# Performance work log

Measured on AMD Instinct MI355X. Metric: run time of the kernel, lower is better.

## Reference

```python
import jax, jax.numpy as jnp
import numpy as np

D_MODEL = 512
D_ALPHA = 100
D_PH = 80
SCALE = 1.0 / np.sqrt(D_MODEL)


def gru_cell(x, h, Wih, Whh, bih, bhh):
    # PyTorch GRU gate order: r, z, n
    gi = x @ Wih.T + bih
    gh = h @ Whh.T + bhh
    ir, iz, inn = jnp.split(gi, 3, axis=-1)
    hr, hz, hn = jnp.split(gh, 3, axis=-1)
    r = jax.nn.sigmoid(ir + hr)
    z = jax.nn.sigmoid(iz + hz)
    n = jnp.tanh(inn + r * hn)
    return (1.0 - z) * n + z * h


def attend(q, k, v):
    # q: [B,D], k/v: [B,L,D]
    scores = jnp.einsum('bd,bld->bl', q, k) * SCALE
    a = jax.nn.softmax(scores, axis=-1)  # [B,L]
    o = jnp.einsum('bl,bld->bd', a, v)
    return a, o


def setup_inputs() -> dict:
    key = jax.random.key(0)
    ks = jax.random.split(key, 25)
    D = D_MODEL

    def u(k, shape, fan):
        return jax.random.uniform(k, shape, jnp.float32, -1.0, 1.0) / np.sqrt(fan)

    inp = {
        'text': jax.random.randint(ks[0], (256, 128), 0, D_ALPHA),
        'tgt': jax.random.randint(ks[1], (256, 64), 0, D_PH),
        'E_alpha': jax.random.normal(ks[2], (D_ALPHA, D), jnp.float32),
        'enc_Wih_f': u(ks[3], (3 * D, D), D),
        'enc_Whh_f': u(ks[4], (3 * D, D), D),
        'enc_bih_f': u(ks[5], (3 * D,), D),
        'enc_bhh_f': u(ks[6], (3 * D,), D),
        'enc_Wih_b': u(ks[7], (3 * D, D), D),
        'enc_Whh_b': u(ks[8], (3 * D, D), D),
        'enc_bih_b': u(ks[9], (3 * D,), D),
        'enc_bhh_b': u(ks[10], (3 * D,), D),
        'hpost_W': u(ks[11], (D, 2 * D), 2 * D),
        'hpost_b': u(ks[12], (D,), 2 * D),
        'wk_W': u(ks[13], (D, 2 * D), 2 * D),
        'wk_b': u(ks[14], (D,), 2 * D),
        'wv_W': u(ks[15], (D, 2 * D), 2 * D),
        'wv_b': u(ks[16], (D,), 2 * D),
        'E_ph': jax.random.normal(ks[17], (D_PH, D), jnp.float32),
        'dec_Wih': u(ks[18], (3 * D, 2 * D), 2 * D),
        'dec_Whh': u(ks[19], (3 * D, D), D),
        'dec_bih': u(ks[20], (3 * D,), D),
        'dec_bhh': u(ks[21], (3 * D,), D),
        'post_W': u(ks[22], (D_PH, D), D),
        'post_b': u(ks[23], (D_PH,), D),
    }
    return inp


def reference(text, tgt, E_alpha, enc_Wih_f, enc_Whh_f, enc_bih_f, enc_bhh_f,
              enc_Wih_b, enc_Whh_b, enc_bih_b, enc_bhh_b, hpost_W, hpost_b,
              wk_W, wk_b, wv_W, wv_b, E_ph, dec_Wih, dec_Whh, dec_bih,
              dec_bhh, post_W, post_b):
    B, LT = text.shape
    LP = tgt.shape[1]

    # ---- Encoder: bidirectional single-layer GRU (eval: dropout = identity)
    emb = E_alpha[text]                     # [B,LT,D]
    xs = jnp.swapaxes(emb, 0, 1)            # [LT,B,D]
    h0 = jnp.zeros((B, D_MODEL), emb.dtype)

    def mk_step(Wih, Whh, bih, bhh):
        def step(h, x):
            h2 = gru_cell(x, h, Wih, Whh, bih, bhh)
            return h2, h2
        return step

    hF, ysF = jax.lax.scan(mk_step(enc_Wih_f, enc_Whh_f, enc_bih_f, enc_bhh_f), h0, xs)
    hB, ysB = jax.lax.scan(mk_step(enc_Wih_b, enc_Whh_b, enc_bih_b, enc_bhh_b), h0, xs[::-1])
    ysB = ysB[::-1]
    enc_o = jnp.swapaxes(jnp.concatenate([ysF, ysB], axis=-1), 0, 1)  # [B,LT,2D]
    h = jnp.tanh(jnp.concatenate([hF, hB], axis=-1) @ hpost_W.T + hpost_b)  # [B,D]

    k = enc_o @ wk_W.T + wk_b               # [B,LT,D]
    v = enc_o @ wv_W.T + wv_b               # [B,LT,D]

    # ---- initial attention from encoder hidden; eval-mode first token is argmax
    # over tgt[:,0] reshaped to [B,1,1], i.e. always index 0.
    a_sl0, a_o0 = attend(h, k, v)
    dec_i0 = jnp.zeros((B,), jnp.int32)

    def dstep(carry, _):
        hh, a_o, a_sl, dec_i = carry
        e = E_ph[dec_i]                                  # [B,D]
        x = gru_cell(jnp.concatenate([e, a_o], axis=-1), hh,
                     dec_Wih, dec_Whh, dec_bih, dec_bhh)  # [B,D]
        o = x @ post_W.T + post_b                         # [B,D_PH]
        n_sl, n_o = attend(x, k, v)
        nxt = jnp.argmax(o, axis=-1).astype(jnp.int32)
        return (x, n_o, n_sl, nxt), (a_sl, o)

    _, (attn_t, res_t) = jax.lax.scan(dstep, (h, a_o0, a_sl0, dec_i0), None, length=LP)
    attn = jnp.swapaxes(attn_t, 0, 1)        # [B,LP,LT]
    res = jnp.swapaxes(res_t, 0, 1)          # [B,LP,D_PH]
    return attn, res
```

## Files before the change

### kernel.cpp

```cpp
#include <hip/hip_runtime.h>
#include <math.h>

#define B   256
#define LT  128
#define LP  64
#define DM  512
#define D3  1536
#define DPH 80
#define SCALE_F 0.044194173824159216f

__device__ __forceinline__ float dot4(float4 a, float4 b) {
    return a.x*b.x + a.y*b.y + a.z*b.z + a.w*b.w;
}
__device__ __forceinline__ float sigmoidf_(float x) {
    return 1.0f / (1.0f + expf(-x));
}

__global__ __launch_bounds__(256) void precompG_kernel(
    const float* __restrict__ Emb, const float* __restrict__ W,
    const float* __restrict__ bias, float* __restrict__ G,
    int wstride, int woff)
{
    const int n  = blockIdx.x * 256 + threadIdx.x;
    const int r0 = blockIdx.y * 4;
    __shared__ float es[4][DM];
    for (int i = threadIdx.x; i < 4 * DM; i += 256)
        es[i >> 9][i & 511] = Emb[(r0 + (i >> 9)) * DM + (i & 511)];
    __syncthreads();
    float acc[4] = {0.f, 0.f, 0.f, 0.f};
    const float* wr = &W[(size_t)n * wstride + woff];
    for (int j = 0; j < DM; j += 4) {
        float4 w4 = *(const float4*)&wr[j];
        #pragma unroll
        for (int rr = 0; rr < 4; ++rr) {
            float4 e4 = *(const float4*)&es[rr][j];
            acc[rr] += dot4(e4, w4);
        }
    }
    float bv = bias[n];
    #pragma unroll
    for (int rr = 0; rr < 4; ++rr)
        G[(r0 + rr) * D3 + n] = acc[rr] + bv;
}

__global__ __launch_bounds__(256) void enc_step_kernel(
    const float* __restrict__ Gf, const float* __restrict__ Gb,
    const float* __restrict__ Whh_f, const float* __restrict__ Whh_b,
    const float* __restrict__ bhh_f, const float* __restrict__ bhh_b,
    const int* __restrict__ text,
    const float* __restrict__ hF_in, float* __restrict__ hF_out,
    const float* __restrict__ hB_in, float* __restrict__ hB_out,
    float* __restrict__ E, int s)
{
    const int dir = blockIdx.z;
    const int t   = dir ? (LT - 1 - s) : s;
    const int yoff = dir ? DM : 0;
    const float* G   = dir ? Gb : Gf;
    const float* Whh = dir ? Whh_b : Whh_f;
    const float* bhh = dir ? bhh_b : bhh_f;
    const float* hin = dir ? hB_in : hF_in;
    float* hout      = dir ? hB_out : hF_out;

    __shared__ float As[2][32][36];
    __shared__ float Bs[2][96][36];

    const int tid = threadIdx.x;
    const int jj  = tid & 15;
    const int bg  = tid >> 4;
    const int jtile = blockIdx.x * 32;
    const int btile = blockIdx.y * 32;

    float pg[2][2][3], php[2][2];
    #pragma unroll
    for (int m = 0; m < 2; ++m) {
        const int b = btile + bg * 2 + m;
        const int c = text[b * LT + t];
        #pragma unroll
        for (int js = 0; js < 2; ++js) {
            const int j = jtile + jj + 16 * js;
            pg[m][js][0] = G[c * D3 + j];
            pg[m][js][1] = G[c * D3 + DM + j];
            pg[m][js][2] = G[c * D3 + 2 * DM + j];
            php[m][js]   = hin[b * DM + j];
        }
    }

    float acc[2][2][3];
    #pragma unroll
    for (int m = 0; m < 2; ++m)
        #pragma unroll
        for (int js = 0; js < 2; ++js)
            #pragma unroll
            for (int g = 0; g < 3; ++g) acc[m][js][g] = 0.f;

    const int lrow = tid >> 3;
    const int lcol = (tid & 7) * 4;
    size_t wbase[3];
    #pragma unroll
    for (int rr = 0; rr < 3; ++rr)
        wbase[rr] = (size_t)(rr * DM + jtile + lrow) * DM;

    float4 rA  = *(const float4*)&hin[(btile + lrow) * DM + lcol];
    float4 rB0 = *(const float4*)&Whh[wbase[0] + lcol];
    float4 rB1 = *(const float4*)&Whh[wbase[1] + lcol];
    float4 rB2 = *(const float4*)&Whh[wbase[2] + lcol];

    int buf = 0;
    for (int kc = 0; kc < 16; ++kc) {
        *(float4*)&As[buf][lrow][lcol]      = rA;
        *(float4*)&Bs[buf][lrow][lcol]      = rB0;
        *(float4*)&Bs[buf][lrow + 32][lcol] = rB1;
        *(float4*)&Bs[buf][lrow + 64][lcol] = rB2;
        __syncthreads();
        if (kc < 15) {
            const int k0 = (kc + 1) * 32;
            rA  = *(const float4*)&hin[(btile + lrow) * DM + k0 + lcol];
            rB0 = *(const float4*)&Whh[wbase[0] + k0 + lcol];
            rB1 = *(const float4*)&Whh[wbase[1] + k0 + lcol];
            rB2 = *(const float4*)&Whh[wbase[2] + k0 + lcol];
        }
        #pragma unroll
        for (int c4 = 0; c4 < 8; ++c4) {
            float4 av[2], bv[2][3];
            #pragma unroll
            for (int m = 0; m < 2; ++m)
                av[m] = *(float4*)&As[buf][bg * 2 + m][c4 * 4];
            #pragma unroll
            for (int js = 0; js < 2; ++js)
                #pragma unroll
                for (int g = 0; g < 3; ++g)
                    bv[js][g] = *(float4*)&Bs[buf][g * 32 + jj + 16 * js][c4 * 4];
            #pragma unroll
            for (int m = 0; m < 2; ++m)
                #pragma unroll
                for (int js = 0; js < 2; ++js)
                    #pragma unroll
                    for (int g = 0; g < 3; ++g)
                        acc[m][js][g] += dot4(av[m], bv[js][g]);
        }
        buf ^= 1;
    }

    #pragma unroll
    for (int m = 0; m < 2; ++m) {
        const int b = btile + bg * 2 + m;
        #pragma unroll
        for (int js = 0; js < 2; ++js) {
            const int j = jtile + jj + 16 * js;
            float hr = acc[m][js][0] + bhh[j];
            float hz = acc[m][js][1] + bhh[DM + j];
            float hn = acc[m][js][2] + bhh[2 * DM + j];
            float r = sigmoidf_(pg[m][js][0] + hr);
            float z = sigmoidf_(pg[m][js][1] + hz);
            float n = tanhf(pg[m][js][2] + r * hn);
            float hv = (1.f - z) * n + z * php[m][js];
            hout[b * DM + j] = hv;
            E[(size_t)(b * LT + t) * 1024 + yoff + j] = hv;
        }
    }
}

__global__ __launch_bounds__(256) void kv_chunk_kernel(
    const float* __restrict__ E,
    const float* __restrict__ wk, const float* __restrict__ wv,
    const float* __restrict__ kb, const float* __restrict__ vb,
    float* __restrict__ T, int r0)
{
    __shared__ float As[64][36];
    __shared__ float Bk[64][36];
    __shared__ float Bv[64][36];
    const int tid = threadIdx.x;
    const int nn = tid & 15, bb = tid >> 4;
    const int ntile = blockIdx.x * 64;
    const int mtile = blockIdx.y * 64;

    float ak[4][4], av_[4][4];
    #pragma unroll
    for (int m = 0; m < 4; ++m)
        #pragma unroll
        for (int i = 0; i < 4; ++i) { ak[m][i] = 0.f; av_[m][i] = 0.f; }

    const int lrow = tid >> 3;
    const int lcol = (tid & 7) * 4;

    for (int k0 = 0; k0 < 1024; k0 += 32) {
        __syncthreads();
        *(float4*)&As[lrow][lcol] =
            *(const float4*)&E[(size_t)(r0 + mtile + lrow) * 1024 + k0 + lcol];
        *(float4*)&As[lrow + 32][lcol] =
            *(const float4*)&E[(size_t)(r0 + mtile + lrow + 32) * 1024 + k0 + lcol];
        *(float4*)&Bk[lrow][lcol] =
            *(const float4*)&wk[(ntile + lrow) * 1024 + k0 + lcol];
        *(float4*)&Bk[lrow + 32][lcol] =
            *(const float4*)&wk[(ntile + lrow + 32) * 1024 + k0 + lcol];
        *(float4*)&Bv[lrow][lcol] =
            *(const float4*)&wv[(ntile + lrow) * 1024 + k0 + lcol];
        *(float4*)&Bv[lrow + 32][lcol] =
            *(const float4*)&wv[(ntile + lrow + 32) * 1024 + k0 + lcol];
        __syncthreads();
        #pragma unroll
        for (int c4 = 0; c4 < 8; ++c4) {
            float4 a4[4], k4[4], v4[4];
            #pragma unroll
            for (int m = 0; m < 4; ++m) a4[m] = *(float4*)&As[bb + 16 * m][c4 * 4];
            #pragma unroll
            for (int i = 0; i < 4; ++i) {
                k4[i] = *(float4*)&Bk[nn + 16 * i][c4 * 4];
                v4[i] = *(float4*)&Bv[nn + 16 * i][c4 * 4];
            }
            #pragma unroll
            for (int m = 0; m < 4; ++m)
                #pragma unroll
                for (int i = 0; i < 4; ++i) {
                    ak[m][i]  += dot4(a4[m], k4[i]);
                    av_[m][i] += dot4(a4[m], v4[i]);
                }
        }
    }
    #pragma unroll
    for (int m = 0; m < 4; ++m) {
        const int lm = mtile + bb + 16 * m;
        #pragma unroll
        for (int i = 0; i < 4; ++i) {
            const int gn = ntile + nn + 16 * i;
            T[(size_t)lm * 1024 + gn]       = ak[m][i]  + kb[gn];
            T[(size_t)lm * 1024 + DM + gn]  = av_[m][i] + vb[gn];
        }
    }
}

__global__ __launch_bounds__(256) void copy4_kernel(
    float4* __restrict__ dst, const float4* __restrict__ src, int n4)
{
    int i = blockIdx.x * 256 + threadIdx.x;
    const int stride = gridDim.x * 256;
    for (; i < n4; i += stride) dst[i] = src[i];
}

__global__ __launch_bounds__(256) void hpost_kernel(
    const float* __restrict__ hF, const float* __restrict__ hB,
    const float* __restrict__ W, const float* __restrict__ bias,
    float* __restrict__ out)
{
    const int b = blockIdx.x;
    __shared__ float as_[1024];
    for (int i = threadIdx.x; i < DM; i += 256) {
        as_[i]      = hF[b * DM + i];
        as_[DM + i] = hB[b * DM + i];
    }
    __syncthreads();
    for (int n = threadIdx.x; n < DM; n += 256) {
        const float* wr = &W[n * 1024];
        float acc = 0.f;
        for (int j = 0; j < 1024; j += 4)
            acc += dot4(*(const float4*)&as_[j], *(const float4*)&wr[j]);
        out[b * DM + n] = tanhf(acc + bias[n]);
    }
}

__global__ __launch_bounds__(256) void dec_step_kernel(
    const float* __restrict__ dec_Wih, const float* __restrict__ dec_Whh,
    const float* __restrict__ a_o, const float* __restrict__ h_in,
    float* __restrict__ P)
{
    const int ph = blockIdx.z;
    const float* Aptr = ph ? h_in : a_o;
    const float* Wsrc = ph ? dec_Whh : dec_Wih;
    const size_t wstride = ph ? 512 : 1024;
    const int woff = ph ? 0 : DM;

    __shared__ float As[2][32][36];
    __shared__ float Bs[2][96][36];

    const int tid = threadIdx.x;
    const int jj  = tid & 15;
    const int bg  = tid >> 4;
    const int jtile = blockIdx.x * 32;
    const int btile = blockIdx.y * 32;

    float acc[2][2][3];
    #pragma unroll
    for (int m = 0; m < 2; ++m)
        #pragma unroll
        for (int js = 0; js < 2; ++js)
            #pragma unroll
            for (int g = 0; g < 3; ++g) acc[m][js][g] = 0.f;

    const int lrow = tid >> 3;
    const int lcol = (tid & 7) * 4;
    size_t wbase[3];
    #pragma unroll
    for (int rr = 0; rr < 3; ++rr)
        wbase[rr] = (size_t)(rr * DM + jtile + lrow) * wstride + woff;

    float4 rA  = *(const float4*)&Aptr[(btile + lrow) * DM + lcol];
    float4 rB0 = *(const float4*)&Wsrc[wbase[0] + lcol];
    float4 rB1 = *(const float4*)&Wsrc[wbase[1] + lcol];
    float4 rB2 = *(const float4*)&Wsrc[wbase[2] + lcol];

    int buf = 0;
    for (int kc = 0; kc < 16; ++kc) {
        *(float4*)&As[buf][lrow][lcol]      = rA;
        *(float4*)&Bs[buf][lrow][lcol]      = rB0;
        *(float4*)&Bs[buf][lrow + 32][lcol] = rB1;
        *(float4*)&Bs[buf][lrow + 64][lcol] = rB2;
        __syncthreads();
        if (kc < 15) {
            const int k0 = (kc + 1) * 32;
            rA  = *(const float4*)&Aptr[(btile + lrow) * DM + k0 + lcol];
            rB0 = *(const float4*)&Wsrc[wbase[0] + k0 + lcol];
            rB1 = *(const float4*)&Wsrc[wbase[1] + k0 + lcol];
            rB2 = *(const float4*)&Wsrc[wbase[2] + k0 + lcol];
        }
        #pragma unroll
        for (int c4 = 0; c4 < 8; ++c4) {
            float4 av[2], bv[2][3];
            #pragma unroll
            for (int m = 0; m < 2; ++m)
                av[m] = *(float4*)&As[buf][bg * 2 + m][c4 * 4];
            #pragma unroll
            for (int js = 0; js < 2; ++js)
                #pragma unroll
                for (int g = 0; g < 3; ++g)
                    bv[js][g] = *(float4*)&Bs[buf][g * 32 + jj + 16 * js][c4 * 4];
            #pragma unroll
            for (int m = 0; m < 2; ++m)
                #pragma unroll
                for (int js = 0; js < 2; ++js)
                    #pragma unroll
                    for (int g = 0; g < 3; ++g)
                        acc[m][js][g] += dot4(av[m], bv[js][g]);
        }
        buf ^= 1;
    }

    float* Pp = P + (size_t)ph * B * 1536;
    #pragma unroll
    for (int m = 0; m < 2; ++m) {
        const int b = btile + bg * 2 + m;
        #pragma unroll
        for (int js = 0; js < 2; ++js) {
            const int j = jtile + jj + 16 * js;
            #pragma unroll
            for (int g = 0; g < 3; ++g)
                Pp[(size_t)b * 1536 + g * 512 + j] = acc[m][js][g];
        }
    }
}

__global__ __launch_bounds__(512) void dec_attend_post_kernel(
    const float* __restrict__ P,
    const float* __restrict__ Gd, const float* __restrict__ dec_bhh,
    const float* __restrict__ h_in, float* __restrict__ h_out,
    const float* __restrict__ q_init,
    const float* __restrict__ EKV,
    const float* __restrict__ post_W, const float* __restrict__ post_b,
    float* __restrict__ attn, float* __restrict__ res,
    float* __restrict__ a_o, int* __restrict__ dec_i,
    int s, int attn_row, int do_combine, int do_post, int do_attn)
{
    const int b = blockIdx.x;
    const int tid = threadIdx.x;
    __shared__ float qs[DM];
    __shared__ float part[512];
    __shared__ float sarr[LT];
    __shared__ float red[2];
    __shared__ float4 pvp[4][128];

    if (do_combine) {
        const int j = tid;
        const int c = dec_i[b];
        const float* P0 = P + (size_t)b * 1536;
        const float* P1 = P + (size_t)B * 1536 + (size_t)b * 1536;
        float rsum = P0[j] + P1[j];
        float zsum = P0[512 + j] + P1[512 + j];
        float r = sigmoidf_(Gd[c * D3 + j] + dec_bhh[j] + rsum);
        float z = sigmoidf_(Gd[c * D3 + DM + j] + dec_bhh[DM + j] + zsum);
        float n = tanhf(Gd[c * D3 + 2 * DM + j] + P0[1024 + j]
                        + r * (P1[1024 + j] + dec_bhh[2 * DM + j]));
        float x = (1.f - z) * n + z * h_in[b * DM + j];
        qs[j] = x;
        h_out[b * DM + j] = x;
    } else if (tid < 128) {
        *(float4*)&qs[tid * 4] = *(const float4*)&q_init[b * DM + tid * 4];
    }
    __syncthreads();

    if (do_post) {
        if (tid < DPH) {
            const float* wr = &post_W[tid * DM];
            float acc = 0.f;
            for (int d = 0; d < DM; d += 4)
                acc += dot4(*(const float4*)&qs[d], *(const float4*)&wr[d]);
            float lv = acc + post_b[tid];
            res[(size_t)(b * LP + s) * DPH + tid] = lv;
            part[tid] = lv;
        }
        __syncthreads();
        if (tid == 0) {
            float best = part[0]; int bi = 0;
            for (int p = 1; p < DPH; ++p) {
                float vv = part[p];
                if (vv > best) { best = vv; bi = p; }
            }
            dec_i[b] = bi;
        }
        __syncthreads();
    }

    if (do_attn) {
        {
            const int r = tid & 127, quad = tid >> 7;
            const float* kr = &EKV[(size_t)(b * LT + r) * 1024 + quad * 128];
            const float* qh = &qs[quad * 128];
            float p0 = 0.f, p1 = 0.f;
            #pragma unroll
            for (int d = 0; d < 128; d += 8) {
                p0 += dot4(*(const float4*)&qh[d],     *(const float4*)&kr[d]);
                p1 += dot4(*(const float4*)&qh[d + 4], *(const float4*)&kr[d + 4]);
            }
            part[tid] = p0 + p1;
        }
        __syncthreads();
        if (tid < LT)
            sarr[tid] = (((part[tid] + part[tid + 128]) + part[tid + 256])
                         + part[tid + 384]) * SCALE_F;
        __syncthreads();
        if (tid < 64) {
            float m = fmaxf(sarr[tid], sarr[tid + 64]);
            #pragma unroll
            for (int off = 32; off > 0; off >>= 1)
                m = fmaxf(m, __shfl_xor(m, off));
            if (tid == 0) red[0] = m;
        }
        __syncthreads();
        const float smax = red[0];
        if (tid < LT) sarr[tid] = expf(sarr[tid] - smax);
        __syncthreads();
        if (tid < 64) {
            float ssum = sarr[tid] + sarr[tid + 64];
            #pragma unroll
            for (int off = 32; off > 0; off >>= 1)
                ssum += __shfl_xor(ssum, off);
            if (tid == 0) red[1] = ssum;
        }
        __syncthreads();
        const float inv = 1.0f / red[1];
        if (tid < LT) {
            float a = sarr[tid] * inv;
            sarr[tid] = a;
            attn[(size_t)(b * LP + attn_row) * LT + tid] = a;
        }
        __syncthreads();
        {
            const int d4 = tid & 127, quad = tid >> 7;
            const float* vb0 = &EKV[(size_t)b * LT * 1024 + DM];
            float4 a0 = make_float4(0.f, 0.f, 0.f, 0.f);
            float4 a1 = make_float4(0.f, 0.f, 0.f, 0.f);
            const int l0 = quad * 32;
            #pragma unroll
            for (int l = l0; l < l0 + 32; l += 2) {
                float w0 = sarr[l], w1 = sarr[l + 1];
                float4 v0 = *(const float4*)&vb0[(size_t)l * 1024 + d4 * 4];
                float4 v1 = *(const float4*)&vb0[(size_t)(l + 1) * 1024 + d4 * 4];
                a0.x += w0 * v0.x; a0.y += w0 * v0.y;
                a0.z += w0 * v0.z; a0.w += w0 * v0.w;
                a1.x += w1 * v1.x; a1.y += w1 * v1.y;
                a1.z += w1 * v1.z; a1.w += w1 * v1.w;
            }
            pvp[quad][d4] = make_float4(a0.x + a1.x, a0.y + a1.y,
                                        a0.z + a1.z, a0.w + a1.w);
        }
        __syncthreads();
        if (tid < 128) {
            float4 p0 = pvp[0][tid], p1 = pvp[1][tid];
            float4 p2 = pvp[2][tid], p3 = pvp[3][tid];
            float4 o = make_float4(((p0.x + p1.x) + p2.x) + p3.x,
                                   ((p0.y + p1.y) + p2.y) + p3.y,
                                   ((p0.z + p1.z) + p2.z) + p3.z,
                                   ((p0.w + p1.w) + p2.w) + p3.w);
            *(float4*)&a_o[b * DM + tid * 4] = o;
        }
    }
}

extern "C" void kernel_launch(void* const* d_in, const int* in_sizes, int n_in,
                              void* d_out, int out_size, void* d_ws, size_t ws_size,
                              hipStream_t stream)
{
    const int*   text    = (const int*)d_in[0];
    const float* E_alpha = (const float*)d_in[2];
    const float* Wih_f   = (const float*)d_in[3];
    const float* Whh_f   = (const float*)d_in[4];
    const float* bih_f   = (const float*)d_in[5];
    const float* bhh_f   = (const float*)d_in[6];
    const float* Wih_b   = (const float*)d_in[7];
    const float* Whh_b   = (const float*)d_in[8];
    const float* bih_b   = (const float*)d_in[9];
    const float* bhh_b   = (const float*)d_in[10];
    const float* hpost_W = (const float*)d_in[11];
    const float* hpost_b = (const float*)d_in[12];
    const float* wk_W    = (const float*)d_in[13];
    const float* wk_b    = (const float*)d_in[14];
    const float* wv_W    = (const float*)d_in[15];
    const float* wv_b    = (const float*)d_in[16];
    const float* E_ph    = (const float*)d_in[17];
    const float* dec_Wih = (const float*)d_in[18];
    const float* dec_Whh = (const float*)d_in[19];
    const float* dec_bih = (const float*)d_in[20];
    const float* dec_bhh = (const float*)d_in[21];
    const float* post_W  = (const float*)d_in[22];
    const float* post_b  = (const float*)d_in[23];

    float* ws = (float*)d_ws;
    float* Gf  = ws;
    float* Gb  = Gf  + 153600;
    float* Gd  = Gb  + 153600;
    float* hF0 = Gd  + 122880;
    float* hF1 = hF0 + 131072;
    float* hB0 = hF1 + 131072;
    float* hB1 = hB0 + 131072;
    float* hd0 = hB1 + 131072;
    float* hd1 = hd0 + 131072;
    float* a_o = hd1 + 131072;
    int*   dec_i = (int*)(a_o + 131072);
    float* P   = a_o + 131072 + 512;
    float* E   = P + 786432;
    float* T   = E + 33554432;

    hipMemsetAsync(hF0, 0, 131072 * sizeof(float), stream);
    hipMemsetAsync(hB0, 0, 131072 * sizeof(float), stream);
    hipMemsetAsync(dec_i, 0, B * sizeof(int), stream);

    precompG_kernel<<<dim3(6, 25), 256, 0, stream>>>(E_alpha, Wih_f, bih_f, Gf, DM, 0);
    precompG_kernel<<<dim3(6, 25), 256, 0, stream>>>(E_alpha, Wih_b, bih_b, Gb, DM, 0);
    precompG_kernel<<<dim3(6, 20), 256, 0, stream>>>(E_ph, dec_Wih, dec_bih, Gd, 1024, 0);

    for (int s = 0; s < LT; ++s) {
        const float* fin = (s & 1) ? hF1 : hF0;
        float*       fou = (s & 1) ? hF0 : hF1;
        const float* bin = (s & 1) ? hB1 : hB0;
        float*       bou = (s & 1) ? hB0 : hB1;
        enc_step_kernel<<<dim3(16, 8, 2), 256, 0, stream>>>(
            Gf, Gb, Whh_f, Whh_b, bhh_f, bhh_b, text,
            fin, fou, bin, bou, E, s);
    }

    for (int c = 0; c < 2; ++c) {
        const int r0 = c * 16384;
        kv_chunk_kernel<<<dim3(8, 256), 256, 0, stream>>>(
            E, wk_W, wv_W, wk_b, wv_b, T, r0);
        copy4_kernel<<<dim3(4096), 256, 0, stream>>>(
            (float4*)(E + (size_t)r0 * 1024), (const float4*)T,
            16384 * 1024 / 4);
    }

    hpost_kernel<<<dim3(B), 256, 0, stream>>>(hF0, hB0, hpost_W, hpost_b, hd0);

    float* attn = (float*)d_out;
    float* res  = attn + (size_t)B * LP * LT;

    dec_attend_post_kernel<<<dim3(B), 512, 0, stream>>>(
        P, Gd, dec_bhh, hd0, hd1, hd0, E, post_W, post_b,
        attn, res, a_o, dec_i,
        0, 0, 0, 0, 1);

    for (int s = 0; s < LP; ++s) {
        const float* hin = (s & 1) ? hd1 : hd0;
        float*       hou = (s & 1) ? hd0 : hd1;
        dec_step_kernel<<<dim3(16, 8, 2), 256, 0, stream>>>(
            dec_Wih, dec_Whh, a_o, hin, P);
        dec_attend_post_kernel<<<dim3(B), 512, 0, stream>>>(
            P, Gd, dec_bhh, hin, hou, hd0 , E, post_W, post_b,
            attn, res, a_o, dec_i,
            s, s + 1, 1, 1, (s < LP - 1) ? 1 : 0);
    }
}
```

Measured before the change: 10.31 ms.

## Enlarge KV projection M-tile to 128 and coalesce decoder score dot products

```diff
diff --git a/kernel.cpp b/kernel.cpp
--- a/kernel.cpp
+++ b/kernel.cpp
@@ -166,17 +166,17 @@
     const float* __restrict__ kb, const float* __restrict__ vb,
     float* __restrict__ T, int r0)
 {
-    __shared__ float As[64][36];
+    __shared__ float As[128][36];
     __shared__ float Bk[64][36];
     __shared__ float Bv[64][36];
     const int tid = threadIdx.x;
     const int nn = tid & 15, bb = tid >> 4;
     const int ntile = blockIdx.x * 64;
-    const int mtile = blockIdx.y * 64;
-
-    float ak[4][4], av_[4][4];
-    #pragma unroll
-    for (int m = 0; m < 4; ++m)
+    const int mtile = blockIdx.y * 128;
+
+    float ak[8][4], av_[8][4];
+    #pragma unroll
+    for (int m = 0; m < 8; ++m)
         #pragma unroll
         for (int i = 0; i < 4; ++i) { ak[m][i] = 0.f; av_[m][i] = 0.f; }
 
@@ -185,10 +185,10 @@
 
     for (int k0 = 0; k0 < 1024; k0 += 32) {
         __syncthreads();
-        *(float4*)&As[lrow][lcol] =
-            *(const float4*)&E[(size_t)(r0 + mtile + lrow) * 1024 + k0 + lcol];
-        *(float4*)&As[lrow + 32][lcol] =
-            *(const float4*)&E[(size_t)(r0 + mtile + lrow + 32) * 1024 + k0 + lcol];
+        #pragma unroll
+        for (int q = 0; q < 4; ++q)
+            *(float4*)&As[lrow + 32 * q][lcol] =
+                *(const float4*)&E[(size_t)(r0 + mtile + lrow + 32 * q) * 1024 + k0 + lcol];
         *(float4*)&Bk[lrow][lcol] =
             *(const float4*)&wk[(ntile + lrow) * 1024 + k0 + lcol];
         *(float4*)&Bk[lrow + 32][lcol] =
@@ -200,16 +200,16 @@
         __syncthreads();
         #pragma unroll
         for (int c4 = 0; c4 < 8; ++c4) {
-            float4 a4[4], k4[4], v4[4];
-            #pragma unroll
-            for (int m = 0; m < 4; ++m) a4[m] = *(float4*)&As[bb + 16 * m][c4 * 4];
+            float4 a4[8], k4[4], v4[4];
+            #pragma unroll
+            for (int m = 0; m < 8; ++m) a4[m] = *(float4*)&As[bb + 16 * m][c4 * 4];
             #pragma unroll
             for (int i = 0; i < 4; ++i) {
                 k4[i] = *(float4*)&Bk[nn + 16 * i][c4 * 4];
                 v4[i] = *(float4*)&Bv[nn + 16 * i][c4 * 4];
             }
             #pragma unroll
-            for (int m = 0; m < 4; ++m)
+            for (int m = 0; m < 8; ++m)
                 #pragma unroll
                 for (int i = 0; i < 4; ++i) {
                     ak[m][i]  += dot4(a4[m], k4[i]);
@@ -218,7 +218,7 @@
         }
     }
     #pragma unroll
-    for (int m = 0; m < 4; ++m) {
+    for (int m = 0; m < 8; ++m) {
         const int lm = mtile + bb + 16 * m;
         #pragma unroll
         for (int i = 0; i < 4; ++i) {
@@ -410,21 +410,25 @@
 
     if (do_attn) {
         {
-            const int r = tid & 127, quad = tid >> 7;
-            const float* kr = &EKV[(size_t)(b * LT + r) * 1024 + quad * 128];
-            const float* qh = &qs[quad * 128];
-            float p0 = 0.f, p1 = 0.f;
-            #pragma unroll
-            for (int d = 0; d < 128; d += 8) {
-                p0 += dot4(*(const float4*)&qh[d],     *(const float4*)&kr[d]);
-                p1 += dot4(*(const float4*)&qh[d + 4], *(const float4*)&kr[d + 4]);
+            const int wave = tid >> 6, lane = tid & 63;
+            const int rl = lane >> 3, dlane = lane & 7;
+            #pragma unroll
+            for (int pass = 0; pass < 2; ++pass) {
+                const int r = pass * 64 + wave * 8 + rl;
+                const float* kr = &EKV[(size_t)(b * LT + r) * 1024];
+                float p = 0.f;
+                #pragma unroll
+                for (int i = 0; i < 16; ++i) {
+                    float4 kv4 = *(const float4*)&kr[dlane * 4 + i * 32];
+                    float4 qv4 = *(const float4*)&qs[dlane * 4 + i * 32];
+                    p += dot4(qv4, kv4);
+                }
+                p += __shfl_xor(p, 1);
+                p += __shfl_xor(p, 2);
+                p += __shfl_xor(p, 4);
+                if (dlane == 0) sarr[r] = p * SCALE_F;
             }
-            part[tid] = p0 + p1;
-        }
-        __syncthreads();
-        if (tid < LT)
-            sarr[tid] = (((part[tid] + part[tid + 128]) + part[tid + 256])
-                         + part[tid + 384]) * SCALE_F;
+        }
         __syncthreads();
         if (tid < 64) {
             float m = fmaxf(sarr[tid], sarr[tid + 64]);
@@ -548,7 +552,7 @@
 
     for (int c = 0; c < 2; ++c) {
         const int r0 = c * 16384;
-        kv_chunk_kernel<<<dim3(8, 256), 256, 0, stream>>>(
+        kv_chunk_kernel<<<dim3(8, 128), 256, 0, stream>>>(
             E, wk_W, wv_W, wk_b, wv_b, T, r0);
         copy4_kernel<<<dim3(4096), 256, 0, stream>>>(
             (float4*)(E + (size_t)r0 * 1024), (const float4*)T,
```

Result: slower. 11.57 ms (+12.2%).
